# Optimization experiments

Measured on AMD Instinct MI355X. Metric: run time of the kernel, lower is better.

Reference implementation:

```python
import jax, jax.numpy as jnp
import numpy as np

CLASS_NUM = 31
KERNEL_MUL = 2.0
KERNEL_NUM = 5


def setup_inputs() -> dict:
    key = jax.random.key(0)
    k1, k2, k3, k4 = jax.random.split(key, 4)
    S_total, T, D = 4096, 2048, 512
    return {
        "source": jax.random.normal(k1, (S_total, D), jnp.float32),
        "target": jax.random.normal(k2, (T, D), jnp.float32),
        "s_label": jax.random.randint(k3, (S_total,), 0, CLASS_NUM),
        "t_label": jax.random.normal(k4, (T, CLASS_NUM), jnp.float32),
        "num_source_data": 2048,
    }


def _mmd_loss(source, target, s_label, t_label, num_source_data):
    # Slice off the first num_source_data source rows (as in get_loss).
    src = source[num_source_data:]              # [S, D]
    s_lab = s_label[num_source_data:]           # [S]
    t_lab = jnp.argmax(t_label, axis=1)         # [T] hard target labels

    total = jnp.concatenate([src, target], axis=0)   # [N, D]
    # Full pairwise squared L2 distances, computed once and reused per class.
    sq = jnp.sum(total * total, axis=1)
    Dmat = jnp.maximum(sq[:, None] + sq[None, :] - 2.0 * (total @ total.T), 0.0)  # [N, N]

    dt = total.dtype
    loss = jnp.zeros((), dt)
    cnt = jnp.zeros((), dt)
    # Fixed small loop over class ids (mirrors the per-class python loop,
    # but uses masks instead of data-dependent boolean indexing for jit).
    for c in range(CLASS_NUM):
        ms = s_lab == c                          # [S] source mask
        mt = t_lab == c                          # [T] target mask
        m = jnp.concatenate([ms, mt]).astype(dt) # [N] pair membership
        # +1 for source rows, -1 for target rows: SS + TT - ST - TS
        sgn = jnp.concatenate([ms.astype(dt), -mt.astype(dt)])
        n = jnp.sum(m)                           # si + ti
        valid = (jnp.any(ms) & jnp.any(mt)).astype(dt)
        # median-heuristic bandwidth over the masked pairs (diag is 0)
        bw = (m @ Dmat @ m) / jnp.maximum(n * n - n, 1.0)
        bw = jnp.where(bw > 0, bw, 1.0) / (KERNEL_MUL ** (KERNEL_NUM // 2))
        K = sum(jnp.exp(-Dmat / (bw * KERNEL_MUL ** i)) for i in range(KERNEL_NUM))
        # sgn zeros out all entries outside the class-c block structure
        loss = loss + valid * (sgn @ K @ sgn) / jnp.maximum(n * n, 1.0)
        cnt = cnt + valid
    return loss / jnp.maximum(cnt, 1.0)


def reference(source, target, s_label, t_label, num_source_data):
    return _mmd_loss(source, target, s_label, t_label, num_source_data)
```

## Files before the change

kernel.cpp:

```cpp
#include <hip/hip_runtime.h>


#define CMAX 32
#define RCAP 6144
#define PCW 32
#define PAIR_Y 8

typedef __attribute__((ext_vector_type(8)))  short  short8;
typedef __attribute__((ext_vector_type(8)))  unsigned short ushort8;
typedef __attribute__((ext_vector_type(16))) float  float16;

__device__ inline unsigned short f2bf(float x) {
  unsigned u = __float_as_uint(x);
  return (unsigned short)((u + 0x7FFFu + ((u >> 16) & 1u)) >> 16);
}

__global__ __launch_bounds__(256) void k_fused(
    const float* __restrict__ src, const float* __restrict__ tgt,
    const int* __restrict__ slab, const float* __restrict__ tlabel,
    const int* __restrict__ nsd_p,
    int* pc,
    unsigned short* __restrict__ fragbuf,
    float* __restrict__ sqc, float* __restrict__ sgnc,
    int S_total, int T, int D, int C) {
  int lane = threadIdx.x & 63;
  int gwid = (blockIdx.x * 256 + threadIdx.x) >> 6;
  int nwv = (gridDim.x * 256) >> 6;
  int nsd = nsd_p[0];
  int S_use = S_total - nsd;
  int N = S_use + T;

  for (int r = gwid; r < N; r += nwv) {
    int c;
    const float* row;
    bool isSrc = (r < S_use);
    if (isSrc) {
      c = slab[nsd + r];
      row = src + (size_t)(nsd + r) * D;
    } else {
      int t = r - S_use;
      row = tgt + (size_t)t * D;
      float v = (lane < C) ? tlabel[(size_t)t * C + lane] : -3.4e38f;
      int idx = lane;
      for (int o = 32; o > 0; o >>= 1) {
        float ov = __shfl_down(v, o, 64);
        int oi = __shfl_down(idx, o, 64);
        if (ov > v || (ov == v && oi < idx)) { v = ov; idx = oi; }
      }
      c = __shfl(idx, 0, 64);
    }
    const float4* s4 = (const float4*)row;
    int nm = D >> 3;
    float4 v0, v1;
    if (lane < nm) { v0 = s4[lane * 2]; v1 = s4[lane * 2 + 1]; }

    int rk;
    if (lane == 0) rk = atomicAdd(&pc[c * PCW], 1);
    rk = __shfl(rk, 0, 64);
    int p = c * RCAP + rk;
    unsigned short* pb = fragbuf + (size_t)(c * RCAP + (rk & ~31)) * D;
    int row32 = rk & 31;

    float s = 0.f;
    if (lane < nm) {
      s += v0.x * v0.x + v0.y * v0.y + v0.z * v0.z + v0.w * v0.w +
           v1.x * v1.x + v1.y * v1.y + v1.z * v1.z + v1.w * v1.w;
      ushort8 h;
      h[0] = f2bf(v0.x); h[1] = f2bf(v0.y); h[2] = f2bf(v0.z); h[3] = f2bf(v0.w);
      h[4] = f2bf(v1.x); h[5] = f2bf(v1.y); h[6] = f2bf(v1.z); h[7] = f2bf(v1.w);
      int st = lane >> 1, hf = lane & 1;
      *(ushort8*)(pb + st * 512 + (hf * 32 + row32) * 8) = h;
    }
    for (int m = lane + 64; m < nm; m += 64) {
      float4 w0 = s4[m * 2], w1 = s4[m * 2 + 1];
      s += w0.x * w0.x + w0.y * w0.y + w0.z * w0.z + w0.w * w0.w +
           w1.x * w1.x + w1.y * w1.y + w1.z * w1.z + w1.w * w1.w;
      ushort8 h;
      h[0] = f2bf(w0.x); h[1] = f2bf(w0.y); h[2] = f2bf(w0.z); h[3] = f2bf(w0.w);
      h[4] = f2bf(w1.x); h[5] = f2bf(w1.y); h[6] = f2bf(w1.z); h[7] = f2bf(w1.w);
      int st = m >> 1, hf = m & 1;
      *(ushort8*)(pb + st * 512 + (hf * 32 + row32) * 8) = h;
    }
    for (int o = 32; o > 0; o >>= 1) s += __shfl_down(s, o, 64);
    if (lane == 0) {
      sqc[p] = s;
      sgnc[p] = isSrc ? 1.f : -1.f;
      atomicAdd((float*)&pc[(CMAX + c) * PCW], s);
      int* flag = &pc[(2 * CMAX + c) * PCW + (isSrc ? 0 : 1)];
      if (*(volatile int*)flag == 0) atomicExch(flag, 1);
    }
  }
}

__global__ __launch_bounds__(256) void k_pairs(
    const unsigned short* __restrict__ fragbuf, const float* __restrict__ sqc,
    const float* __restrict__ sgnc, const int* __restrict__ pc,
    float* losssum, int* done, float* __restrict__ out, int D, int C) {
  __shared__ float scs[4][64][8];
  __shared__ float s_inv0;
  __shared__ int lastFlag;
  int c = blockIdx.x;
  int tid = threadIdx.x;
  int n = pc[c * PCW];
  int off = c * RCAP;
  const unsigned short* base = fragbuf + (size_t)off * D;
  int nm = D >> 3;

  int rg = tid >> 6, cl = tid & 63;
  float nspart = 0.f;
  for (int m0 = 0; m0 < nm; m0 += 64) {
    int m = m0 + cl;
    float cs[8] = {0.f, 0.f, 0.f, 0.f, 0.f, 0.f, 0.f, 0.f};
    if (m < nm) {
      int st = m >> 1, hf = m & 1;
      for (int i = rg; i < n; i += 4) {
        ushort8 v = *(const ushort8*)(base + (size_t)(i & ~31) * D +
                                      st * 512 + (hf * 32 + (i & 31)) * 8);
        #pragma unroll
        for (int j = 0; j < 8; j++)
          cs[j] += __uint_as_float((unsigned)v[j] << 16);
      }
    }
    #pragma unroll
    for (int j = 0; j < 8; j++) scs[rg][cl][j] = cs[j];
    __syncthreads();
    if (tid < 64) {
      #pragma unroll
      for (int j = 0; j < 8; j++) {
        float t = scs[0][tid][j] + scs[1][tid][j] +
                  scs[2][tid][j] + scs[3][tid][j];
        nspart += t * t;
      }
    }
    __syncthreads();
  }
  if (tid < 64) {
    for (int o = 32; o > 0; o >>= 1) nspart += __shfl_down(nspart, o, 64);
    if (tid == 0) {
      float ss = ((const float*)pc)[(CMAX + c) * PCW];
      float nf = (float)n;
      float S1 = 2.f * nf * ss - 2.f * nspart;
      float bw = S1 / fmaxf(nf * nf - nf, 1.f);
      bw = (bw > 0.f) ? bw : 1.f;
      s_inv0 = 4.f / bw;
    }
  }
  __syncthreads();
  float inv0 = s_inv0;

  int tpr = (n + 31) >> 5;
  int tiles = tpr * (tpr + 1) / 2;
  int lane = tid & 63, l31 = lane & 31, half = lane >> 5;
  int wvc = blockIdx.y * 4 + (tid >> 6);
  int nwvc = gridDim.y * 4;
  float wsum = 0.f;

  for (int t = wvc; t < tiles; t += nwvc) {
    int lt = t, jt = 0;
    while (lt >= tpr - jt) { lt -= tpr - jt; jt++; }
    int kt = jt + lt;
    int jbase = jt << 5, kbase = kt << 5;
    float wgt = (jt == kt) ? 1.f : 2.f;

    const unsigned short* fa  = fragbuf + (size_t)(off + jbase) * D + lane * 8;
    const unsigned short* fbp = fragbuf + (size_t)(off + kbase) * D + lane * 8;
    float16 acc = {};
    if (D == 512) {
      #pragma unroll
      for (int s = 0; s < 32; s++) {
        short8 a = *(const short8*)(fa + s * 512);
        short8 b = *(const short8*)(fbp + s * 512);
        acc = __builtin_amdgcn_mfma_f32_32x32x16_bf16(a, b, acc, 0, 0, 0);
      }
    } else {
      for (int s = 0; s < (D >> 4); s++) {
        short8 a = *(const short8*)(fa + s * 512);
        short8 b = *(const short8*)(fbp + s * 512);
        acc = __builtin_amdgcn_mfma_f32_32x32x16_bf16(a, b, acc, 0, 0, 0);
      }
    }

    float sqk = sqc[off + kbase + l31];
    float sgk = sgnc[off + kbase + l31];
    bool kval = (kbase + l31) < n;
    float sqjv = sqc[off + jbase + l31];
    float sgjv = sgnc[off + jbase + l31];
    float contrib = 0.f;
    #pragma unroll
    for (int r = 0; r < 16; r++) {
      int m = (r & 3) + 8 * (r >> 2) + 4 * half;
      float sqj = __shfl(sqjv, m, 64);
      float sgj = __shfl(sgjv, m, 64);
      if (kval && (jbase + m) < n) {
        float d = fmaxf(sqj + sqk - 2.f * acc[r], 0.f);
        float s = inv0, kv = 0.f;
        #pragma unroll
        for (int q = 0; q < 5; q++) { kv += __expf(-d * s); s *= 0.5f; }
        contrib += sgj * sgk * kv;
      }
    }
    wsum += wgt * contrib;
  }
  for (int o = 32; o > 0; o >>= 1) wsum += __shfl_down(wsum, o, 64);
  if (lane == 0 && wsum != 0.f) atomicAdd(&losssum[c], wsum);

  __syncthreads();
  if (tid == 0) {
    __threadfence();
    int d = atomicAdd(done, 1);
    lastFlag = (d == (int)(gridDim.x * gridDim.y) - 1);
  }
  __syncthreads();
  if (lastFlag && tid < 64) {
    int cc = tid;
    float loss = 0.f, cv = 0.f;
    if (cc < C && pc[(2 * CMAX + cc) * PCW] > 0 &&
        pc[(2 * CMAX + cc) * PCW + 1] > 0) {
      float nf = (float)pc[cc * PCW];
      loss = atomicAdd(&losssum[cc], 0.f) / fmaxf(nf * nf, 1.f);
      cv = 1.f;
    }
    for (int o = 32; o > 0; o >>= 1) {
      loss += __shfl_down(loss, o, 64);
      cv   += __shfl_down(cv, o, 64);
    }
    if (tid == 0) out[0] = loss / fmaxf(cv, 1.f);
  }
}

extern "C" void kernel_launch(void* const* d_in, const int* in_sizes, int n_in,
                              void* d_out, int out_size, void* d_ws, size_t ws_size,
                              hipStream_t stream) {
  const float* source = (const float*)d_in[0];
  const float* target = (const float*)d_in[1];
  const int* slab     = (const int*)d_in[2];
  const float* tlabel = (const float*)d_in[3];
  const int* nsd_p    = (const int*)d_in[4];
  float* out = (float*)d_out;

  int S_total = in_sizes[2];
  int D = in_sizes[0] / S_total;
  int T = in_sizes[1] / D;
  int C = in_sizes[3] / T;

  int* ws = (int*)d_ws;
  int* pc       = ws;
  float* losssum = (float*)(ws + 3 * CMAX * PCW);
  int* done     = (int*)(losssum + C);
  int zwords    = 3 * CMAX * PCW + C + 8;

  float* sqc    = (float*)(ws + zwords);
  float* sgnc   = sqc + (size_t)C * RCAP;
  size_t words_used = (size_t)zwords + 2 * (size_t)C * RCAP;
  size_t fw = (words_used + 63) & ~(size_t)63;
  unsigned short* fragbuf = (unsigned short*)(ws + fw);

  hipMemsetAsync(d_ws, 0, (size_t)zwords * sizeof(int), stream);

  k_fused<<<1024, 256, 0, stream>>>(source, target, slab, tlabel, nsd_p,
                                    pc, fragbuf, sqc, sgnc,
                                    S_total, T, D, C);
  k_pairs<<<dim3(C, PAIR_Y), 256, 0, stream>>>(fragbuf, sqc, sgnc, pc,
                                               losssum, done, out, D, C);
}
```

Baseline: 99.93 us.

## Offload per-class bandwidth reduction to one block, overlap MFMA tiles via flag

Before this change every pair block redundantly computed the per-class column-sum and bandwidth before starting its tiles. Now only blockIdx.y==0 does that reduction and publishes inv0 through a release-store flag. The other WY blocks start their MFMA tile work right away and spin on the flag only when they reach the exponential stage. It also shortens the argmax shuffle reduction to 32 lanes, turns the flag write into a plain store, and hoists the sq/sign loads above the MFMA loop. The spin-wait relies on block y==0 being co-resident or already scheduled, which risks deadlock or stalls if the grid ever exceeds what the GPU can hold at once.

After: 105.1 us. 1.05x slower.

```diff
diff --git a/kernel.cpp b/kernel.cpp
--- a/kernel.cpp
+++ b/kernel.cpp
@@ -4,7 +4,7 @@
 #define CMAX 32
 #define RCAP 6144
 #define PCW 32
-#define PAIR_Y 8
+#define WY 8
 
 typedef __attribute__((ext_vector_type(8)))  short  short8;
 typedef __attribute__((ext_vector_type(8)))  unsigned short ushort8;
@@ -42,7 +42,7 @@
       row = tgt + (size_t)t * D;
       float v = (lane < C) ? tlabel[(size_t)t * C + lane] : -3.4e38f;
       int idx = lane;
-      for (int o = 32; o > 0; o >>= 1) {
+      for (int o = 16; o > 0; o >>= 1) {
         float ov = __shfl_down(v, o, 64);
         int oi = __shfl_down(idx, o, 64);
         if (ov > v || (ov == v && oi < idx)) { v = ov; idx = oi; }
@@ -86,8 +86,7 @@
       sqc[p] = s;
       sgnc[p] = isSrc ? 1.f : -1.f;
       atomicAdd((float*)&pc[(CMAX + c) * PCW], s);
-      int* flag = &pc[(2 * CMAX + c) * PCW + (isSrc ? 0 : 1)];
-      if (*(volatile int*)flag == 0) atomicExch(flag, 1);
+      pc[(2 * CMAX + c) * PCW + (isSrc ? 0 : 1)] = 1;
     }
   }
 }
@@ -95,64 +94,67 @@
 __global__ __launch_bounds__(256) void k_pairs(
     const unsigned short* __restrict__ fragbuf, const float* __restrict__ sqc,
     const float* __restrict__ sgnc, const int* __restrict__ pc,
-    float* losssum, int* done, float* __restrict__ out, int D, int C) {
+    int* bws, float* losssum, int* done, float* __restrict__ out,
+    int D, int C) {
   __shared__ float scs[4][64][8];
-  __shared__ float s_inv0;
   __shared__ int lastFlag;
-  int c = blockIdx.x;
+  int c = blockIdx.x, y = blockIdx.y;
   int tid = threadIdx.x;
   int n = pc[c * PCW];
   int off = c * RCAP;
   const unsigned short* base = fragbuf + (size_t)off * D;
   int nm = D >> 3;
 
-  int rg = tid >> 6, cl = tid & 63;
-  float nspart = 0.f;
-  for (int m0 = 0; m0 < nm; m0 += 64) {
-    int m = m0 + cl;
-    float cs[8] = {0.f, 0.f, 0.f, 0.f, 0.f, 0.f, 0.f, 0.f};
-    if (m < nm) {
-      int st = m >> 1, hf = m & 1;
-      for (int i = rg; i < n; i += 4) {
-        ushort8 v = *(const ushort8*)(base + (size_t)(i & ~31) * D +
-                                      st * 512 + (hf * 32 + (i & 31)) * 8);
+  if (y == 0) {
+    int rg = tid >> 6, cl = tid & 63;
+    float nspart = 0.f;
+    for (int m0 = 0; m0 < nm; m0 += 64) {
+      int m = m0 + cl;
+      float cs[8] = {0.f, 0.f, 0.f, 0.f, 0.f, 0.f, 0.f, 0.f};
+      if (m < nm) {
+        int st = m >> 1, hf = m & 1;
+        for (int i = rg; i < n; i += 4) {
+          ushort8 v = *(const ushort8*)(base + (size_t)(i & ~31) * D +
+                                        st * 512 + (hf * 32 + (i & 31)) * 8);
+          #pragma unroll
+          for (int j = 0; j < 8; j++)
+            cs[j] += __uint_as_float((unsigned)v[j] << 16);
+        }
+      }
+      #pragma unroll
+      for (int j = 0; j < 8; j++) scs[rg][cl][j] = cs[j];
+      __syncthreads();
+      if (tid < 64) {
         #pragma unroll
-        for (int j = 0; j < 8; j++)
-          cs[j] += __uint_as_float((unsigned)v[j] << 16);
-      }
-    }
-    #pragma unroll
-    for (int j = 0; j < 8; j++) scs[rg][cl][j] = cs[j];
-    __syncthreads();
+        for (int j = 0; j < 8; j++) {
+          float t = scs[0][tid][j] + scs[1][tid][j] +
+                    scs[2][tid][j] + scs[3][tid][j];
+          nspart += t * t;
+        }
+      }
+      __syncthreads();
+    }
     if (tid < 64) {
-      #pragma unroll
-      for (int j = 0; j < 8; j++) {
-        float t = scs[0][tid][j] + scs[1][tid][j] +
-                  scs[2][tid][j] + scs[3][tid][j];
-        nspart += t * t;
-      }
-    }
-    __syncthreads();
-  }
-  if (tid < 64) {
-    for (int o = 32; o > 0; o >>= 1) nspart += __shfl_down(nspart, o, 64);
-    if (tid == 0) {
-      float ss = ((const float*)pc)[(CMAX + c) * PCW];
-      float nf = (float)n;
-      float S1 = 2.f * nf * ss - 2.f * nspart;
-      float bw = S1 / fmaxf(nf * nf - nf, 1.f);
-      bw = (bw > 0.f) ? bw : 1.f;
-      s_inv0 = 4.f / bw;
-    }
-  }
-  __syncthreads();
-  float inv0 = s_inv0;
+      for (int o = 32; o > 0; o >>= 1) nspart += __shfl_down(nspart, o, 64);
+      if (tid == 0) {
+        float ss = ((const float*)pc)[(CMAX + c) * PCW];
+        float nf = (float)n;
+        float S1 = 2.f * nf * ss - 2.f * nspart;
+        float bw = S1 / fmaxf(nf * nf - nf, 1.f);
+        bw = (bw > 0.f) ? bw : 1.f;
+        float inv0 = 4.f / bw;
+        __hip_atomic_store(bws + c * PCW, __float_as_int(inv0),
+                           __ATOMIC_RELEASE, __HIP_MEMORY_SCOPE_AGENT);
+      }
+    }
+  }
 
   int tpr = (n + 31) >> 5;
   int tiles = tpr * (tpr + 1) / 2;
   int lane = tid & 63, l31 = lane & 31, half = lane >> 5;
-  int wvc = blockIdx.y * 4 + (tid >> 6);
-  int nwvc = gridDim.y * 4;
+  int wvc = (y == 0) ? (4 * WY + (tid >> 6)) : ((y - 1) * 4 + (tid >> 6));
+  int nwvc = 4 * WY + 4;
+  float inv0 = -1.f;
   float wsum = 0.f;
 
   for (int t = wvc; t < tiles; t += nwvc) {
@@ -161,6 +163,12 @@
     int kt = jt + lt;
     int jbase = jt << 5, kbase = kt << 5;
     float wgt = (jt == kt) ? 1.f : 2.f;
+
+    float sqk  = sqc[off + kbase + l31];
+    float sgk  = sgnc[off + kbase + l31];
+    float sqjv = sqc[off + jbase + l31];
+    float sgjv = sgnc[off + jbase + l31];
+    bool kval = (kbase + l31) < n;
 
     const unsigned short* fa  = fragbuf + (size_t)(off + jbase) * D + lane * 8;
     const unsigned short* fbp = fragbuf + (size_t)(off + kbase) * D + lane * 8;
@@ -180,11 +188,21 @@
       }
     }
 
-    float sqk = sqc[off + kbase + l31];
-    float sgk = sgnc[off + kbase + l31];
-    bool kval = (kbase + l31) < n;
-    float sqjv = sqc[off + jbase + l31];
-    float sgjv = sgnc[off + jbase + l31];
+    if (inv0 < 0.f) {
+      int v;
+      if (lane == 0) {
+        v = __hip_atomic_load(bws + c * PCW, __ATOMIC_ACQUIRE,
+                              __HIP_MEMORY_SCOPE_AGENT);
+        while (v == 0) {
+          __builtin_amdgcn_s_sleep(2);
+          v = __hip_atomic_load(bws + c * PCW, __ATOMIC_ACQUIRE,
+                                __HIP_MEMORY_SCOPE_AGENT);
+        }
+      }
+      v = __shfl(v, 0, 64);
+      inv0 = __int_as_float(v);
+    }
+
     float contrib = 0.f;
     #pragma unroll
     for (int r = 0; r < 16; r++) {
@@ -245,9 +263,10 @@
 
   int* ws = (int*)d_ws;
   int* pc       = ws;
-  float* losssum = (float*)(ws + 3 * CMAX * PCW);
+  int* bws      = ws + 3 * CMAX * PCW;
+  float* losssum = (float*)(ws + 4 * CMAX * PCW);
   int* done     = (int*)(losssum + C);
-  int zwords    = 3 * CMAX * PCW + C + 8;
+  int zwords    = 4 * CMAX * PCW + C + 8;
 
   float* sqc    = (float*)(ws + zwords);
   float* sgnc   = sqc + (size_t)C * RCAP;
@@ -260,6 +279,6 @@
   k_fused<<<1024, 256, 0, stream>>>(source, target, slab, tlabel, nsd_p,
                                     pc, fragbuf, sqc, sgnc,
                                     S_total, T, D, C);
-  k_pairs<<<dim3(C, PAIR_Y), 256, 0, stream>>>(fragbuf, sqc, sgnc, pc,
-                                               losssum, done, out, D, C);
-}
+  k_pairs<<<dim3(C, 1 + WY), 256, 0, stream>>>(fragbuf, sqc, sgnc, pc,
+                                               bws, losssum, done, out, D, C);
+}
```
